# Kernel tuning notes

Hardware: AMD Instinct MI355X
Metric: run time of the kernel (lower is better)

Reference implementation:

```python
import jax, jax.numpy as jnp
import numpy as np

N = 50000       # nodes
E = 800000      # edges (before self-loops)
G = 64          # graphs in batch
F_IN = 128      # node_features
HID = 64        # hidden_channels
H1 = 8          # conv1 heads
NEG_SLOPE = 0.2
EPS = 1e-16


def _gat_layer(x, src, dst, W, att_src, att_dst, bias, heads, out_ch, concat):
    """PyG GATConv (eval mode: dropout inactive). src/dst include self-loops.
    x: [N, F_in]; W: [F_in, heads*out_ch]; att_*: [heads, out_ch]; bias: [heads*out_ch] or [out_ch]."""
    n = x.shape[0]
    h = (x @ W).reshape(n, heads, out_ch)                 # [N,H,C]
    a_s = jnp.sum(h * att_src, axis=-1)                   # [N,H]
    a_d = jnp.sum(h * att_dst, axis=-1)                   # [N,H]
    e = jax.nn.leaky_relu(a_s[src] + a_d[dst], NEG_SLOPE)  # [Etot,H]
    # segment softmax over incoming edges of each destination node
    m = jax.ops.segment_max(e, dst, num_segments=n)       # [N,H]
    e = jnp.exp(e - m[dst])
    denom = jax.ops.segment_sum(e, dst, num_segments=n)   # [N,H]
    alpha = e / (denom[dst] + EPS)                        # [Etot,H]
    msg = h[src] * alpha[:, :, None]                      # [Etot,H,C]
    out = jax.ops.segment_sum(msg, dst, num_segments=n)   # [N,H,C]
    if concat:
        out = out.reshape(n, heads * out_ch)
    else:
        out = out.mean(axis=1)
    return out + bias


def setup_inputs() -> dict:
    key = jax.random.key(0)
    ks = jax.random.split(key, 14)
    x = jax.random.normal(ks[0], (N, F_IN), dtype=jnp.float32)
    edge_index = jax.random.randint(ks[1], (2, E), 0, N, dtype=jnp.int64)
    batch_index = jnp.sort(jax.random.randint(ks[2], (N,), 0, G, dtype=jnp.int64))
    s = 0.05
    return {
        "x": x,
        "edge_index": edge_index,
        "batch_index": batch_index,
        "W1": jax.random.normal(ks[3], (F_IN, H1 * HID), dtype=jnp.float32) * s,
        "att_src1": jax.random.normal(ks[4], (H1, HID), dtype=jnp.float32) * s,
        "att_dst1": jax.random.normal(ks[5], (H1, HID), dtype=jnp.float32) * s,
        "b1": jnp.zeros((H1 * HID,), dtype=jnp.float32),
        "W2": jax.random.normal(ks[6], (H1 * HID, HID), dtype=jnp.float32) * s,
        "att_src2": jax.random.normal(ks[7], (1, HID), dtype=jnp.float32) * s,
        "att_dst2": jax.random.normal(ks[8], (1, HID), dtype=jnp.float32) * s,
        "b2": jnp.zeros((HID,), dtype=jnp.float32),
        "lin_W": jax.random.normal(ks[9], (HID, 1), dtype=jnp.float32) * s,
        "lin_b": jnp.zeros((1,), dtype=jnp.float32),
    }


def reference(x, edge_index, batch_index, W1, att_src1, att_dst1, b1,
              W2, att_src2, att_dst2, b2, lin_W, lin_b):
    n = x.shape[0]
    loops = jnp.arange(n, dtype=edge_index.dtype)
    src = jnp.concatenate([edge_index[0], loops])
    dst = jnp.concatenate([edge_index[1], loops])
    # eval mode: F.dropout is identity
    h = jax.nn.elu(_gat_layer(x, src, dst, W1, att_src1, att_dst1, b1, H1, HID, True))
    h = _gat_layer(h, src, dst, W2, att_src2, att_dst2, b2, 1, HID, False)
    # global mean pool over graphs
    sums = jax.ops.segment_sum(h, batch_index, num_segments=G)          # [G,HID]
    cnt = jax.ops.segment_sum(jnp.ones((n,), h.dtype), batch_index, num_segments=G)
    pooled = sums / jnp.maximum(cnt, 1.0)[:, None]
    return pooled @ lin_W + lin_b                                       # [G,1]
```

## Files before the change

kernel.cpp:

```cpp
#include <hip/hip_runtime.h>
#include <math.h>

#define NN 50000
#define EE 800000
#define ET 850000
#define GG 64
#define MPAD 50048
#define NCAP 64
#define NROW 50016
#define CSRI (NROW * NCAP)
#define CSTRIDE 32

typedef __attribute__((ext_vector_type(8))) short bf16x8;
typedef __attribute__((ext_vector_type(4))) float f32x4;

__device__ __forceinline__ float lrelu(float v) { return v > 0.f ? v : 0.2f * v; }

__device__ __forceinline__ unsigned short f2bf(float f) {
  unsigned u = __float_as_uint(f);
  u += 0x7FFFu + ((u >> 16) & 1u);
  return (unsigned short)(u >> 16);
}
__device__ __forceinline__ unsigned pack2(float a, float b) {
  return (unsigned)f2bf(a) | ((unsigned)f2bf(b) << 16);
}
__device__ __forceinline__ void bfacc4(uint4 u, float a, float* o) {
  o[0] += a * __uint_as_float(u.x << 16);
  o[1] += a * __uint_as_float(u.x & 0xFFFF0000u);
  o[2] += a * __uint_as_float(u.y << 16);
  o[3] += a * __uint_as_float(u.y & 0xFFFF0000u);
  o[4] += a * __uint_as_float(u.z << 16);
  o[5] += a * __uint_as_float(u.z & 0xFFFF0000u);
  o[6] += a * __uint_as_float(u.w << 16);
  o[7] += a * __uint_as_float(u.w & 0xFFFF0000u);
}

#define INIT_BLOCKS 1563
#define CVT_X_BLOCKS 3128
#define CVT_W_BLOCKS 256
#define V_BLOCKS 2
#define GSEG_BLOCKS 196
__global__ __launch_bounds__(256) void prep_kernel(const float* __restrict__ x,
                                                   const float* __restrict__ W1,
                                                   const float* __restrict__ W2,
                                                   const float* __restrict__ att_s2,
                                                   const float* __restrict__ att_d2,
                                                   const float* __restrict__ linW,
                                                   const int* __restrict__ batch,
                                                   unsigned short* __restrict__ xb,
                                                   unsigned short* __restrict__ W1T,
                                                   float* __restrict__ Vs,
                                                   float* __restrict__ Vd,
                                                   float* __restrict__ Vz,
                                                   int* __restrict__ gstart,
                                                   int* __restrict__ cursor,
                                                   unsigned short* __restrict__ csr) {
  int b = blockIdx.x;
  if (b < INIT_BLOCKS) {
    int i = b * 256 + threadIdx.x;
    if (i < CSRI / 8) {
      uint4 sf = {0xC350C350u, 0xC350C350u, 0xC350C350u, 0xC350C350u};
      ((uint4*)csr)[i] = sf;
    }
    if (i < NROW) cursor[i * CSTRIDE] = 0;
  } else if (b < INIT_BLOCKS + CVT_X_BLOCKS) {
    int i8 = (b - INIT_BLOCKS) * 256 + threadIdx.x;
    if (i8 >= MPAD * 128 / 8) return;
    size_t e0 = (size_t)i8 * 8;
    int row = (int)(e0 >> 7);
    uint4 o;
    if (row < NN) {
      float4 f0 = *(const float4*)(x + e0);
      float4 f1 = *(const float4*)(x + e0 + 4);
      o.x = pack2(f0.x, f0.y); o.y = pack2(f0.z, f0.w);
      o.z = pack2(f1.x, f1.y); o.w = pack2(f1.z, f1.w);
    } else {
      o.x = o.y = o.z = o.w = 0u;
    }
    *(uint4*)(xb + e0) = o;
  } else if (b < INIT_BLOCKS + CVT_X_BLOCKS + CVT_W_BLOCKS) {
    int i = (b - INIT_BLOCKS - CVT_X_BLOCKS) * 256 + threadIdx.x;
    int k = i >> 9, n = i & 511;
    W1T[n * 128 + k] = f2bf(W1[i]);
  } else if (b < INIT_BLOCKS + CVT_X_BLOCKS + CVT_W_BLOCKS + V_BLOCKS) {
    int k = (b - INIT_BLOCKS - CVT_X_BLOCKS - CVT_W_BLOCKS) * 256 + threadIdx.x;
    float vs = 0.f, vd = 0.f, vz = 0.f;
#pragma unroll 8
    for (int c = 0; c < 64; ++c) {
      float w = W2[k * 64 + c];
      vs += w * att_s2[c];
      vd += w * att_d2[c];
      vz += w * linW[c];
    }
    Vs[k] = vs; Vd[k] = vd; Vz[k] = vz;
  } else {
    int e = (b - INIT_BLOCKS - CVT_X_BLOCKS - CVT_W_BLOCKS - V_BLOCKS) * 256 + threadIdx.x;
    if (e < NN) {
      int bb = batch[e];
      if (e == 0) {
        for (int g = 0; g <= bb; ++g) gstart[g] = 0;
      } else {
        int pb = batch[e - 1];
        for (int g = pb + 1; g <= bb; ++g) gstart[g] = e;
      }
      if (e == NN - 1) {
        for (int g = bb + 1; g <= GG; ++g) gstart[g] = NN;
      }
    }
  }
}

#define GEMM_BLOCKS 3128
#define SCAT_BLOCKS 831
#define SCAT_STRIDE (SCAT_BLOCKS * 256)
__global__ __launch_bounds__(256) void gemm1_scatter(const unsigned short* __restrict__ xb,
                                                     const unsigned short* __restrict__ W1T,
                                                     const float* __restrict__ att_s,
                                                     const float* __restrict__ att_d,
                                                     unsigned short* __restrict__ h1b,
                                                     float* __restrict__ as1,
                                                     float* __restrict__ ad1,
                                                     const int* __restrict__ ei,
                                                     int* __restrict__ cursor,
                                                     unsigned short* __restrict__ csr) {
  __shared__ unsigned short st[2][64 * 72];
  const int idx = blockIdx.x;
  const bool is_scat = ((idx & 3) == 3) && ((idx >> 2) < SCAT_BLOCKS);
  if (is_scat) {
    int base = (idx >> 2) * 256 + threadIdx.x;
#pragma unroll
    for (int k = 0; k < 4; ++k) {
      int e = base + k * SCAT_STRIDE;
      if (e < ET) {
        int src = (e < EE) ? ei[e] : (e - EE);
        int dst = (e < EE) ? ei[EE + e] : (e - EE);
        int pos = atomicAdd(&cursor[dst * CSTRIDE], 1);
        if (pos < NCAP) csr[dst * NCAP + pos] = (unsigned short)src;
      }
    }
    return;
  }
  const int gi = idx - min((idx + 1) >> 2, SCAT_BLOCKS);

  const int t = threadIdx.x, w = t >> 6, l = t & 63;
  const int bm = (gi >> 2) * 64;
  const int ypair = gi & 3;
  const int m16 = l & 15, q = l >> 4;
  const int row = bm + w * 16 + m16;

  const bf16x8* Ap = (const bf16x8*)(xb + (size_t)row * 128 + q * 8);
  bf16x8 a0 = Ap[0], a1 = Ap[4], a2 = Ap[8], a3 = Ap[12];

  const int r2 = t >> 2, c16 = (t & 3) * 16;

#pragma unroll
  for (int hh = 0; hh < 2; ++hh) {
    const int h = ypair * 2 + hh;
    const bf16x8* Bp = (const bf16x8*)(W1T + (size_t)(h * 64 + m16) * 128 + q * 8);
    f32x4 acc[4] = {};
#pragma unroll
    for (int c = 0; c < 4; ++c) {
      acc[c] = __builtin_amdgcn_mfma_f32_16x16x32_bf16(a0, Bp[(size_t)c * 256 + 0],  acc[c], 0, 0, 0);
      acc[c] = __builtin_amdgcn_mfma_f32_16x16x32_bf16(a1, Bp[(size_t)c * 256 + 4],  acc[c], 0, 0, 0);
      acc[c] = __builtin_amdgcn_mfma_f32_16x16x32_bf16(a2, Bp[(size_t)c * 256 + 8],  acc[c], 0, 0, 0);
      acc[c] = __builtin_amdgcn_mfma_f32_16x16x32_bf16(a3, Bp[(size_t)c * 256 + 12], acc[c], 0, 0, 0);
    }

    float ps[4] = {0.f, 0.f, 0.f, 0.f}, pd[4] = {0.f, 0.f, 0.f, 0.f};
#pragma unroll
    for (int c = 0; c < 4; ++c) {
      float ws = att_s[h * 64 + m16 + 16 * c];
      float wd = att_d[h * 64 + m16 + 16 * c];
#pragma unroll
      for (int r = 0; r < 4; ++r) {
        ps[r] += acc[c][r] * ws;
        pd[r] += acc[c][r] * wd;
      }
    }
#pragma unroll
    for (int off = 1; off < 16; off <<= 1) {
#pragma unroll
      for (int r = 0; r < 4; ++r) {
        ps[r] += __shfl_xor(ps[r], off);
        pd[r] += __shfl_xor(pd[r], off);
      }
    }
    if (m16 == 0) {
#pragma unroll
      for (int r = 0; r < 4; ++r) {
        int rr = bm + w * 16 + q * 4 + r;
        as1[rr * 8 + h] = (rr < NN) ? ps[r] : -1e30f;
        ad1[rr * 8 + h] = (rr < NN) ? pd[r] : 0.f;
      }
    }

#pragma unroll
    for (int c = 0; c < 4; ++c)
#pragma unroll
      for (int r = 0; r < 4; ++r)
        st[hh][(w * 16 + q * 4 + r) * 72 + m16 + 16 * c] = f2bf(acc[c][r]);
    __syncthreads();
    uint4* dst = (uint4*)(h1b + (size_t)(bm + r2) * 512 + h * 64 + c16);
    const uint4* srcp = (const uint4*)(st[hh] + r2 * 72 + c16);
    dst[0] = srcp[0];
    dst[1] = srcp[1];
  }
}

__global__ __launch_bounds__(256) void agg1_kernel(const unsigned short* __restrict__ h1b,
                                                   const float* __restrict__ as1,
                                                   const float* __restrict__ ad1,
                                                   const int* __restrict__ cnt,
                                                   const unsigned short* __restrict__ csr,
                                                   const float* __restrict__ b1,
                                                   const float* __restrict__ Vs,
                                                   const float* __restrict__ Vd,
                                                   const float* __restrict__ Vz,
                                                   float* __restrict__ as2,
                                                   float* __restrict__ ad2,
                                                   float* __restrict__ zz) {
  int dst = blockIdx.x * 4 + (threadIdx.x >> 6);
  int lane = threadIdx.x & 63;
  if (dst >= NN) return;
  const int s = dst * NCAP;
  const int e = s + ((cnt[dst * CSTRIDE] + 7) & ~7);
  const int ha = lane >> 3;
  const int hb = ha * 8;
  const int slot_a = lane & 7;
  const float adv_a = ad1[dst * 8 + ha];

  float den = 0.f;
  float o[8] = {0.f, 0.f, 0.f, 0.f, 0.f, 0.f, 0.f, 0.f};
  for (int i = s; i < e; i += 8) {
    uint4 cc = *(const uint4*)(csr + i);
    int s0 = cc.x & 0xFFFF, s1 = (int)(cc.x >> 16);
    int s2 = cc.y & 0xFFFF, s3 = (int)(cc.y >> 16);
    int s4 = cc.z & 0xFFFF, s5 = (int)(cc.z >> 16);
    int s6 = cc.w & 0xFFFF, s7 = (int)(cc.w >> 16);
    unsigned pr = (slot_a & 4) ? ((slot_a & 2) ? cc.w : cc.z)
                               : ((slot_a & 2) ? cc.y : cc.x);
    int my_src = (slot_a & 1) ? (int)(pr >> 16) : (int)(pr & 0xFFFF);
    float myal = __expf(lrelu(as1[my_src * 8 + ha] + adv_a));

    uint4 u0 = *(const uint4*)(h1b + (size_t)s0 * 512 + lane * 8);
    uint4 u1 = *(const uint4*)(h1b + (size_t)s1 * 512 + lane * 8);
    uint4 u2 = *(const uint4*)(h1b + (size_t)s2 * 512 + lane * 8);
    uint4 u3 = *(const uint4*)(h1b + (size_t)s3 * 512 + lane * 8);
    uint4 u4 = *(const uint4*)(h1b + (size_t)s4 * 512 + lane * 8);
    uint4 u5 = *(const uint4*)(h1b + (size_t)s5 * 512 + lane * 8);
    uint4 u6 = *(const uint4*)(h1b + (size_t)s6 * 512 + lane * 8);
    uint4 u7 = *(const uint4*)(h1b + (size_t)s7 * 512 + lane * 8);
    float a0 = __shfl(myal, hb + 0), a1 = __shfl(myal, hb + 1);
    float a2 = __shfl(myal, hb + 2), a3 = __shfl(myal, hb + 3);
    float a4 = __shfl(myal, hb + 4), a5 = __shfl(myal, hb + 5);
    float a6 = __shfl(myal, hb + 6), a7 = __shfl(myal, hb + 7);
    den += ((a0 + a1) + (a2 + a3)) + ((a4 + a5) + (a6 + a7));
    bfacc4(u0, a0, o); bfacc4(u1, a1, o);
    bfacc4(u2, a2, o); bfacc4(u3, a3, o);
    bfacc4(u4, a4, o); bfacc4(u5, a5, o);
    bfacc4(u6, a6, o); bfacc4(u7, a7, o);
  }
  float inv = 1.0f / (den + 1e-16f);

  const float4* bp = (const float4*)(b1 + lane * 8);
  float4 bb0 = bp[0], bb1 = bp[1];
  float bb[8] = {bb0.x, bb0.y, bb0.z, bb0.w, bb1.x, bb1.y, bb1.z, bb1.w};
  float v[8];
#pragma unroll
  for (int j = 0; j < 8; ++j) {
    float t = o[j] * inv + bb[j];
    v[j] = (t > 0.f) ? t : (__expf(t) - 1.0f);
  }

  const float4* vsp = (const float4*)(Vs + lane * 8);
  const float4* vdp = (const float4*)(Vd + lane * 8);
  const float4* vzp = (const float4*)(Vz + lane * 8);
  float4 vs0 = vsp[0], vs1 = vsp[1];
  float4 vd0 = vdp[0], vd1 = vdp[1];
  float4 vz0 = vzp[0], vz1 = vzp[1];
  float ps = v[0]*vs0.x + v[1]*vs0.y + v[2]*vs0.z + v[3]*vs0.w
           + v[4]*vs1.x + v[5]*vs1.y + v[6]*vs1.z + v[7]*vs1.w;
  float pd = v[0]*vd0.x + v[1]*vd0.y + v[2]*vd0.z + v[3]*vd0.w
           + v[4]*vd1.x + v[5]*vd1.y + v[6]*vd1.z + v[7]*vd1.w;
  float pz = v[0]*vz0.x + v[1]*vz0.y + v[2]*vz0.z + v[3]*vz0.w
           + v[4]*vz1.x + v[5]*vz1.y + v[6]*vz1.z + v[7]*vz1.w;
#pragma unroll
  for (int off = 1; off < 64; off <<= 1) {
    ps += __shfl_xor(ps, off);
    pd += __shfl_xor(pd, off);
    pz += __shfl_xor(pz, off);
  }
  if (lane == 0) {
    as2[dst] = ps;
    ad2[dst] = pd;
    zz[dst]  = pz;
  }
}

__global__ __launch_bounds__(256) void agg2z_kernel(const float* __restrict__ as2,
                                                    const float* __restrict__ ad2,
                                                    const float* __restrict__ z,
                                                    const int* __restrict__ cnt,
                                                    const unsigned short* __restrict__ csr,
                                                    float* __restrict__ s) {
  int dst = blockIdx.x * 4 + (threadIdx.x >> 6);
  int lane = threadIdx.x & 63;
  if (dst >= NN) return;
  const int si = dst * NCAP, e = si + cnt[dst * CSTRIDE];
  const float adv = ad2[dst];
  float num = 0.f, den = 0.f;
  for (int i = si + lane; i < e; i += 64) {
    int src = csr[i];
    float a = __expf(lrelu(as2[src] + adv));
    num += a * z[src];
    den += a;
  }
#pragma unroll
  for (int off = 32; off > 0; off >>= 1) {
    num += __shfl_xor(num, off);
    den += __shfl_xor(den, off);
  }
  if (lane == 0) s[dst] = num / (den + 1e-16f);
}

__global__ __launch_bounds__(256) void poolz_kernel(const float* __restrict__ s,
                                                    const int* __restrict__ gstart,
                                                    const float* __restrict__ b2,
                                                    const float* __restrict__ linW,
                                                    const float* __restrict__ linb,
                                                    float* __restrict__ out) {
  __shared__ float red[4];
  int g = blockIdx.x;
  int t = threadIdx.x, lane = t & 63, w = t >> 6;
  int s0 = gstart[g], e0 = gstart[g + 1];
  float acc = 0.f;
  for (int i = s0 + t; i < e0; i += 256) acc += s[i];
#pragma unroll
  for (int off = 32; off > 0; off >>= 1) acc += __shfl_xor(acc, off);
  if (lane == 0) red[w] = acc;
  __syncthreads();
  if (w == 0) {
    float total = red[0] + red[1] + red[2] + red[3];
    float bz = b2[lane] * linW[lane];
#pragma unroll
    for (int off = 32; off > 0; off >>= 1) bz += __shfl_xor(bz, off);
    if (lane == 0) {
      float cnt = fmaxf((float)(e0 - s0), 1.0f);
      out[g] = total / cnt + bz + linb[0];
    }
  }
}

extern "C" void kernel_launch(void* const* d_in, const int* in_sizes, int n_in,
                              void* d_out, int out_size, void* d_ws, size_t ws_size,
                              hipStream_t stream) {
  const float* x      = (const float*)d_in[0];
  const int*   ei     = (const int*)d_in[1];
  const int*   batch  = (const int*)d_in[2];
  const float* W1     = (const float*)d_in[3];
  const float* att_s1 = (const float*)d_in[4];
  const float* att_d1 = (const float*)d_in[5];
  const float* b1     = (const float*)d_in[6];
  const float* W2     = (const float*)d_in[7];
  const float* att_s2 = (const float*)d_in[8];
  const float* att_d2 = (const float*)d_in[9];
  const float* b2     = (const float*)d_in[10];
  const float* linW   = (const float*)d_in[11];
  const float* linb   = (const float*)d_in[12];
  float* out = (float*)d_out;

  char* base = (char*)d_ws;
  unsigned short* xb  = (unsigned short*)base; base += (size_t)MPAD * 128 * 2;
  unsigned short* h1b = (unsigned short*)base; base += (size_t)MPAD * 512 * 2;
  unsigned short* W1T = (unsigned short*)base; base += (size_t)512 * 128 * 2;
  float* Vs   = (float*)base; base += (size_t)512 * 4;
  float* Vd   = (float*)base; base += (size_t)512 * 4;
  float* Vz   = (float*)base; base += (size_t)512 * 4;
  float* as1  = (float*)base; base += (size_t)MPAD * 8 * 4;
  float* ad1  = (float*)base; base += (size_t)MPAD * 8 * 4;
  float* as2  = (float*)base; base += (size_t)NROW * 4;
  float* ad2  = (float*)base; base += (size_t)NROW * 4;
  float* zz   = (float*)base; base += (size_t)NROW * 4;
  float* sv   = (float*)base; base += (size_t)NROW * 4;
  int* cursor = (int*)base;  base += (size_t)NROW * CSTRIDE * 4;
  unsigned short* csr = (unsigned short*)base; base += (size_t)CSRI * 2;
  int* gstart = (int*)base;  base += (size_t)(GG + 16) * 4;

  if (ws_size < (size_t)(base - (char*)d_ws)) return;

  prep_kernel<<<INIT_BLOCKS + CVT_X_BLOCKS + CVT_W_BLOCKS + V_BLOCKS + GSEG_BLOCKS,
                256, 0, stream>>>(x, W1, W2, att_s2, att_d2, linW, batch,
                                  xb, W1T, Vs, Vd, Vz, gstart, cursor, csr);

  gemm1_scatter<<<GEMM_BLOCKS + SCAT_BLOCKS, 256, 0, stream>>>(
      xb, W1T, att_s1, att_d1, h1b, as1, ad1, ei, cursor, csr);

  agg1_kernel<<<12500, 256, 0, stream>>>(h1b, as1, ad1, cursor, csr, b1,
                                         Vs, Vd, Vz, as2, ad2, zz);

  agg2z_kernel<<<12500, 256, 0, stream>>>(as2, ad2, zz, cursor, csr, sv);
  poolz_kernel<<<GG, 256, 0, stream>>>(sv, gstart, b2, linW, linb, out);
}
```

Baseline: 310.0 us.

## Double-buffer neighbor gathers in agg1 and preload CSR row via shuffles

```diff
diff --git a/kernel.cpp b/kernel.cpp
--- a/kernel.cpp
+++ b/kernel.cpp
@@ -207,58 +207,86 @@
   }
 }
 
-__global__ __launch_bounds__(256) void agg1_kernel(const unsigned short* __restrict__ h1b,
-                                                   const float* __restrict__ as1,
-                                                   const float* __restrict__ ad1,
-                                                   const int* __restrict__ cnt,
-                                                   const unsigned short* __restrict__ csr,
-                                                   const float* __restrict__ b1,
-                                                   const float* __restrict__ Vs,
-                                                   const float* __restrict__ Vd,
-                                                   const float* __restrict__ Vz,
-                                                   float* __restrict__ as2,
-                                                   float* __restrict__ ad2,
-                                                   float* __restrict__ zz) {
+__device__ __forceinline__ void issue8(const unsigned short* __restrict__ h1b,
+                                       const float* __restrict__ as1,
+                                       const uint4 cb, int k, int lane,
+                                       int slot_a, int ha,
+                                       uint4* u, float& asv) {
+  uint4 cc;
+  cc.x = __shfl(cb.x, k);
+  cc.y = __shfl(cb.y, k);
+  cc.z = __shfl(cb.z, k);
+  cc.w = __shfl(cb.w, k);
+  unsigned pr = (slot_a & 4) ? ((slot_a & 2) ? cc.w : cc.z)
+                             : ((slot_a & 2) ? cc.y : cc.x);
+  int my_src = (slot_a & 1) ? (int)(pr >> 16) : (int)(pr & 0xFFFFu);
+  asv = as1[my_src * 8 + ha];
+  int s0 = (int)(cc.x & 0xFFFFu), s1 = (int)(cc.x >> 16);
+  int s2 = (int)(cc.y & 0xFFFFu), s3 = (int)(cc.y >> 16);
+  int s4 = (int)(cc.z & 0xFFFFu), s5 = (int)(cc.z >> 16);
+  int s6 = (int)(cc.w & 0xFFFFu), s7 = (int)(cc.w >> 16);
+  u[0] = *(const uint4*)(h1b + (size_t)s0 * 512 + lane * 8);
+  u[1] = *(const uint4*)(h1b + (size_t)s1 * 512 + lane * 8);
+  u[2] = *(const uint4*)(h1b + (size_t)s2 * 512 + lane * 8);
+  u[3] = *(const uint4*)(h1b + (size_t)s3 * 512 + lane * 8);
+  u[4] = *(const uint4*)(h1b + (size_t)s4 * 512 + lane * 8);
+  u[5] = *(const uint4*)(h1b + (size_t)s5 * 512 + lane * 8);
+  u[6] = *(const uint4*)(h1b + (size_t)s6 * 512 + lane * 8);
+  u[7] = *(const uint4*)(h1b + (size_t)s7 * 512 + lane * 8);
+}
+
+__device__ __forceinline__ void proc8(const uint4* u, float asv, float adv,
+                                      int hb, float* o, float& den) {
+  float myal = __expf(lrelu(asv + adv));
+  float a0 = __shfl(myal, hb + 0), a1 = __shfl(myal, hb + 1);
+  float a2 = __shfl(myal, hb + 2), a3 = __shfl(myal, hb + 3);
+  float a4 = __shfl(myal, hb + 4), a5 = __shfl(myal, hb + 5);
+  float a6 = __shfl(myal, hb + 6), a7 = __shfl(myal, hb + 7);
+  den += ((a0 + a1) + (a2 + a3)) + ((a4 + a5) + (a6 + a7));
+  bfacc4(u[0], a0, o); bfacc4(u[1], a1, o);
+  bfacc4(u[2], a2, o); bfacc4(u[3], a3, o);
+  bfacc4(u[4], a4, o); bfacc4(u[5], a5, o);
+  bfacc4(u[6], a6, o); bfacc4(u[7], a7, o);
+}
+
+__global__ __launch_bounds__(256, 4) void agg1_kernel(const unsigned short* __restrict__ h1b,
+                                                      const float* __restrict__ as1,
+                                                      const float* __restrict__ ad1,
+                                                      const int* __restrict__ cnt,
+                                                      const unsigned short* __restrict__ csr,
+                                                      const float* __restrict__ b1,
+                                                      const float* __restrict__ Vs,
+                                                      const float* __restrict__ Vd,
+                                                      const float* __restrict__ Vz,
+                                                      float* __restrict__ as2,
+                                                      float* __restrict__ ad2,
+                                                      float* __restrict__ zz) {
   int dst = blockIdx.x * 4 + (threadIdx.x >> 6);
   int lane = threadIdx.x & 63;
   if (dst >= NN) return;
-  const int s = dst * NCAP;
-  const int e = s + ((cnt[dst * CSTRIDE] + 7) & ~7);
   const int ha = lane >> 3;
   const int hb = ha * 8;
   const int slot_a = lane & 7;
+
+  const int cv = min(cnt[dst * CSTRIDE], NCAP);
+  const uint4 cb = *(const uint4*)(csr + dst * NCAP + (lane & 7) * 8);
   const float adv_a = ad1[dst * 8 + ha];
+  const int nb = (cv + 7) >> 3;
 
   float den = 0.f;
   float o[8] = {0.f, 0.f, 0.f, 0.f, 0.f, 0.f, 0.f, 0.f};
-  for (int i = s; i < e; i += 8) {
-    uint4 cc = *(const uint4*)(csr + i);
-    int s0 = cc.x & 0xFFFF, s1 = (int)(cc.x >> 16);
-    int s2 = cc.y & 0xFFFF, s3 = (int)(cc.y >> 16);
-    int s4 = cc.z & 0xFFFF, s5 = (int)(cc.z >> 16);
-    int s6 = cc.w & 0xFFFF, s7 = (int)(cc.w >> 16);
-    unsigned pr = (slot_a & 4) ? ((slot_a & 2) ? cc.w : cc.z)
-                               : ((slot_a & 2) ? cc.y : cc.x);
-    int my_src = (slot_a & 1) ? (int)(pr >> 16) : (int)(pr & 0xFFFF);
-    float myal = __expf(lrelu(as1[my_src * 8 + ha] + adv_a));
-
-    uint4 u0 = *(const uint4*)(h1b + (size_t)s0 * 512 + lane * 8);
-    uint4 u1 = *(const uint4*)(h1b + (size_t)s1 * 512 + lane * 8);
-    uint4 u2 = *(const uint4*)(h1b + (size_t)s2 * 512 + lane * 8);
-    uint4 u3 = *(const uint4*)(h1b + (size_t)s3 * 512 + lane * 8);
-    uint4 u4 = *(const uint4*)(h1b + (size_t)s4 * 512 + lane * 8);
-    uint4 u5 = *(const uint4*)(h1b + (size_t)s5 * 512 + lane * 8);
-    uint4 u6 = *(const uint4*)(h1b + (size_t)s6 * 512 + lane * 8);
-    uint4 u7 = *(const uint4*)(h1b + (size_t)s7 * 512 + lane * 8);
-    float a0 = __shfl(myal, hb + 0), a1 = __shfl(myal, hb + 1);
-    float a2 = __shfl(myal, hb + 2), a3 = __shfl(myal, hb + 3);
-    float a4 = __shfl(myal, hb + 4), a5 = __shfl(myal, hb + 5);
-    float a6 = __shfl(myal, hb + 6), a7 = __shfl(myal, hb + 7);
-    den += ((a0 + a1) + (a2 + a3)) + ((a4 + a5) + (a6 + a7));
-    bfacc4(u0, a0, o); bfacc4(u1, a1, o);
-    bfacc4(u2, a2, o); bfacc4(u3, a3, o);
-    bfacc4(u4, a4, o); bfacc4(u5, a5, o);
-    bfacc4(u6, a6, o); bfacc4(u7, a7, o);
+  uint4 uA[8], uB[8];
+  float asA, asB;
+
+  issue8(h1b, as1, cb, 0, lane, slot_a, ha, uA, asA);
+  int k = 0;
+  for (;;) {
+    if (k + 1 < nb) issue8(h1b, as1, cb, k + 1, lane, slot_a, ha, uB, asB);
+    proc8(uA, asA, adv_a, hb, o, den);
+    if (++k >= nb) break;
+    if (k + 1 < nb) issue8(h1b, as1, cb, k + 1, lane, slot_a, ha, uA, asA);
+    proc8(uB, asB, adv_a, hb, o, den);
+    if (++k >= nb) break;
   }
   float inv = 1.0f / (den + 1e-16f);
 
```

After: 386.3 us. 24.6% more time.
